# Kernel optimization log

Hardware: AMD Instinct MI355X
Metric: run time of the kernel (lower is better)

Reference implementation:

```python
import jax, jax.numpy as jnp
import numpy as np

HEADS = 8
DIM_HEAD = 64
SCALE = DIM_HEAD ** -0.5


def setup_inputs() -> dict:
    key = jax.random.key(0)
    ks = jax.random.split(key, 7)
    b, n, m = 2, 4096, 4096
    query_dim, context_dim, inner = 1024, 768, HEADS * DIM_HEAD
    s = 0.02
    return {
        "x": jax.random.normal(ks[0], (b, n, query_dim), jnp.float32),
        "context": jax.random.normal(ks[1], (b, m, context_dim), jnp.float32),
        "Wq": jax.random.normal(ks[2], (query_dim, inner), jnp.float32) * s,
        "Wk": jax.random.normal(ks[3], (context_dim, inner), jnp.float32) * s,
        "Wv": jax.random.normal(ks[4], (context_dim, inner), jnp.float32) * s,
        "Wo": jax.random.normal(ks[5], (inner, query_dim), jnp.float32) * s,
        "bo": jnp.zeros((query_dim,), jnp.float32),
    }


def reference(x, context, Wq, Wk, Wv, Wo, bo):
    b, n, _ = x.shape
    m = context.shape[1]
    # projections (no bias), split heads: b n (h d) -> b n h d
    q = (x @ Wq).reshape(b, n, HEADS, DIM_HEAD)
    k = (context @ Wk).reshape(b, m, HEADS, DIM_HEAD)
    v = (context @ Wv).reshape(b, m, HEADS, DIM_HEAD)
    # fp32 QK^T (ATTN_PRECISION='fp32' path), full [b,h,n,m] scores
    sim = jnp.einsum("bihd,bjhd->bhij", q.astype(jnp.float32), k.astype(jnp.float32)) * SCALE
    attn = jax.nn.softmax(sim, axis=-1).astype(v.dtype)
    out = jnp.einsum("bhij,bjhd->bihd", attn, v).reshape(b, n, HEADS * DIM_HEAD)
    # to_out: Linear with bias (dropout=0 is identity)
    return out @ Wo + bo
```

## Files before the change

### kernel.cpp

```cpp
#include <hip/hip_runtime.h>
#include <hip/hip_bf16.h>
#include <cmath>


using bf16_t = __hip_bfloat16;
typedef __bf16 bf16x8 __attribute__((ext_vector_type(8)));
typedef float  f32x4  __attribute__((ext_vector_type(4)));

static constexpr int BATCH = 2;
static constexpr int NQ    = 4096;
static constexpr int NKV   = 4096;
static constexpr int NH    = 8;
static constexpr int DH    = 64;
static constexpr int INNER = NH * DH;
static constexpr int QDIM  = 1024;
static constexpr int CDIM  = 768;
static constexpr float QSCALE = 0.125f * 1.4426950408889634f;

#define MFMA_BF16(a, b, c) __builtin_amdgcn_mfma_f32_16x16x32_bf16((a), (b), (c), 0, 0, 0)

__device__ __forceinline__ float fast_exp2(float x) {
  return __builtin_amdgcn_exp2f(x);
}

__device__ __forceinline__ void gload_lds16(const bf16_t* g, bf16_t* l) {
  __builtin_amdgcn_global_load_lds(
      (const __attribute__((address_space(1))) unsigned int*)(uintptr_t)g,
      (__attribute__((address_space(3))) unsigned int*)(unsigned int)(uintptr_t)l,
      16, 0, 0);
}

__global__ __launch_bounds__(256) void cast_kernel(const float* __restrict__ in,
                                                   bf16_t* __restrict__ out, int n8) {
  int id = blockIdx.x * 256 + threadIdx.x;
  if (id >= n8) return;
  float4 a = ((const float4*)in)[2 * id];
  float4 b = ((const float4*)in)[2 * id + 1];
  bf16_t t[8] = {__float2bfloat16(a.x), __float2bfloat16(a.y), __float2bfloat16(a.z),
                 __float2bfloat16(a.w), __float2bfloat16(b.x), __float2bfloat16(b.y),
                 __float2bfloat16(b.z), __float2bfloat16(b.w)};
  ((uint4*)out)[id] = *(const uint4*)t;
}

__global__ __launch_bounds__(256) void wtrans_kernel(const float* __restrict__ W,
                                                     bf16_t* __restrict__ WT,
                                                     int K, int N) {
  __shared__ float tile[32][33];
  const int bn = blockIdx.x * 32, bk = blockIdx.y * 32;
  const int tx = threadIdx.x & 31, ty = threadIdx.x >> 5;
  for (int yy = ty; yy < 32; yy += 8)
    tile[yy][tx] = W[(size_t)(bk + yy) * N + bn + tx];
  __syncthreads();
  for (int yy = ty; yy < 32; yy += 8)
    WT[(size_t)(bn + yy) * K + bk + tx] = __float2bfloat16(tile[tx][yy]);
}

template <int IM, int OUT_MODE>
__global__ __launch_bounds__(256) void gemm_kernel(const bf16_t* __restrict__ A,
                                                   const bf16_t* __restrict__ WT,
                                                   void* __restrict__ Cp,
                                                   void* __restrict__ Cp2,
                                                   const float* __restrict__ bias,
                                                   float ascale, int M, int N, int K) {
  constexpr int BM = IM * 32;
  __shared__ __align__(16) bf16_t As[BM][32];
  __shared__ __align__(16) bf16_t Bs[128][32];
  const int tid = threadIdx.x;
  const int lane = tid & 63, wave = tid >> 6;
  const int lane15 = lane & 15, quad = lane >> 4;
  const int wm = (wave >> 1) * (BM / 2), wn = (wave & 1) * 64;
  const int m0 = blockIdx.x * BM, n0 = blockIdx.y * 128;

  const f32x4 vzero = {0.f, 0.f, 0.f, 0.f};
  f32x4 acc[IM][4];
  for (int i = 0; i < IM; ++i)
    for (int j = 0; j < 4; ++j) acc[i][j] = vzero;

  const int crow = lane >> 2, ccol = (lane & 3) * 8;
  for (int k0 = 0; k0 < K; k0 += 32) {
    if constexpr (IM == 4) {
      for (int cc = 0; cc < 2; ++cc) {
        int c = wave * 2 + cc;
        gload_lds16(A + (size_t)(m0 + c * 16 + crow) * K + k0 + ccol, &As[c * 16][0]);
        gload_lds16(WT + (size_t)(n0 + c * 16 + crow) * K + k0 + ccol, &Bs[c * 16][0]);
      }
    } else {
      gload_lds16(A + (size_t)(m0 + wave * 16 + crow) * K + k0 + ccol, &As[wave * 16][0]);
      for (int cc = 0; cc < 2; ++cc) {
        int c = wave * 2 + cc;
        gload_lds16(WT + (size_t)(n0 + c * 16 + crow) * K + k0 + ccol, &Bs[c * 16][0]);
      }
    }
    __syncthreads();
    bf16x8 af[IM], bfr[4];
    for (int i = 0; i < IM; ++i)
      af[i] = *reinterpret_cast<const bf16x8*>(&As[wm + i * 16 + lane15][quad * 8]);
    for (int j = 0; j < 4; ++j)
      bfr[j] = *reinterpret_cast<const bf16x8*>(&Bs[wn + j * 16 + lane15][quad * 8]);
    for (int i = 0; i < IM; ++i)
      for (int j = 0; j < 4; ++j) acc[i][j] = MFMA_BF16(af[i], bfr[j], acc[i][j]);
    __syncthreads();
  }

  for (int i = 0; i < IM; ++i) {
    int gm = m0 + wm + i * 16 + quad * 4;
    for (int j = 0; j < 4; ++j) {
      int gn = n0 + wn + j * 16 + lane15;
      for (int r = 0; r < 4; ++r) {
        float v = acc[i][j][r];
        if constexpr (OUT_MODE == 0) {
          ((bf16_t*)Cp)[(size_t)(gm + r) * N + gn] = __float2bfloat16(v * ascale);
        } else if constexpr (OUT_MODE == 1) {
          ((float*)Cp)[(size_t)(gm + r) * N + gn] = v + bias[gn];
        } else {
          if (gn < INNER) {
            ((bf16_t*)Cp)[(size_t)(gm + r) * INNER + gn] = __float2bfloat16(v);
          } else {
            int gmr = gm + r;
            ((bf16_t*)Cp2)[((size_t)(gmr >> 12) * INNER + (gn - INNER)) * (size_t)NKV +
                           (gmr & 4095)] = __float2bfloat16(v);
          }
        }
      }
    }
  }
}

__global__ __launch_bounds__(256) void attn_kernel(const bf16_t* Qg ,
                                                   const bf16_t* __restrict__ Kg ,
                                                   const bf16_t* __restrict__ Vtg ,
                                                   bf16_t* Og ) {
  __shared__ __align__(16) bf16_t KsF[2][8][512];
  __shared__ __align__(16) bf16_t VtF[2][8][512];
  __shared__ __align__(16) bf16_t PsA[128][72];

  const int tid = threadIdx.x;
  const int lane = tid & 63, wave = tid >> 6;
  const int lane15 = lane & 15, quad = lane >> 4;
  const int wrow = wave * 32;
  const int q0 = blockIdx.x * 128;
  const int h = blockIdx.y;
  const int b = blockIdx.z;

  const size_t qbase  = ((size_t)b * NQ + q0) * INNER + h * DH;
  const size_t kbase  = ((size_t)b * NKV) * INNER + h * DH;
  const size_t vtbase = ((size_t)(b * NH + h) * DH) * NKV;

  bf16x8 qf[2][2];
  for (int i = 0; i < 2; ++i)
    for (int ks = 0; ks < 2; ++ks)
      qf[i][ks] = *reinterpret_cast<const bf16x8*>(
          Qg + qbase + (size_t)(wrow + i * 16 + lane15) * INNER + ks * 32 + quad * 8);

  const f32x4 vzero = {0.f, 0.f, 0.f, 0.f};
  f32x4 acc_o[2][4];
  float l_part[2] = {0.f, 0.f};
  for (int i = 0; i < 2; ++i)
    for (int j = 0; j < 4; ++j) acc_o[i][j] = vzero;

  const int c0 = wave * 2, c1 = wave * 2 + 1;
  auto kaddr = [&](int c, int kv0) {
    return Kg + kbase + (size_t)(kv0 + (c & 3) * 16 + lane15) * INNER + (c >> 2) * 32 + quad * 8;
  };
  auto vaddr = [&](int c, int kv0) {
    return Vtg + vtbase + (size_t)((c & 3) * 16 + lane15) * NKV + kv0 + (c >> 2) * 32 + quad * 8;
  };
  uint4 kr0 = *(const uint4*)kaddr(c0, 0), kr1 = *(const uint4*)kaddr(c1, 0);
  uint4 vr0 = *(const uint4*)vaddr(c0, 0), vr1 = *(const uint4*)vaddr(c1, 0);

  constexpr int T = NKV / 64;
  for (int t = 0; t < T; ++t) {
    const int cur = t & 1;
    *(uint4*)&KsF[cur][c0][lane * 8] = kr0;
    *(uint4*)&KsF[cur][c1][lane * 8] = kr1;
    *(uint4*)&VtF[cur][c0][lane * 8] = vr0;
    *(uint4*)&VtF[cur][c1][lane * 8] = vr1;
    __syncthreads();

    f32x4 acc_st[4][2];
    for (int j = 0; j < 4; ++j)
      for (int i = 0; i < 2; ++i) acc_st[j][i] = vzero;
    for (int ks = 0; ks < 2; ++ks) {
      bf16x8 kf[4];
      for (int j = 0; j < 4; ++j)
        kf[j] = *reinterpret_cast<const bf16x8*>(&KsF[cur][ks * 4 + j][lane * 8]);
      for (int j = 0; j < 4; ++j)
        for (int i = 0; i < 2; ++i) acc_st[j][i] = MFMA_BF16(kf[j], qf[i][ks], acc_st[j][i]);
    }

    if (t + 1 < T) {
      int kv0n = (t + 1) * 64;
      kr0 = *(const uint4*)kaddr(c0, kv0n);
      kr1 = *(const uint4*)kaddr(c1, kv0n);
      vr0 = *(const uint4*)vaddr(c0, kv0n);
      vr1 = *(const uint4*)vaddr(c1, kv0n);
    }

    for (int i = 0; i < 2; ++i) {
      for (int j = 0; j < 4; ++j) {
        bf16_t t4[4];
        for (int r = 0; r < 4; ++r) {
          float p = fast_exp2(acc_st[j][i][r]);
          l_part[i] += p;
          t4[r] = __float2bfloat16(p);
        }
        *(uint2*)&PsA[wrow + i * 16 + lane15][j * 16 + quad * 4] = *(const uint2*)t4;
      }
    }
    __syncthreads();

    for (int ks = 0; ks < 2; ++ks) {
      bf16x8 pf[2], vf[4];
      for (int i = 0; i < 2; ++i)
        pf[i] = *reinterpret_cast<const bf16x8*>(&PsA[wrow + i * 16 + lane15][ks * 32 + quad * 8]);
      for (int j = 0; j < 4; ++j)
        vf[j] = *reinterpret_cast<const bf16x8*>(&VtF[cur][ks * 4 + j][lane * 8]);
      for (int i = 0; i < 2; ++i)
        for (int j = 0; j < 4; ++j) acc_o[i][j] = MFMA_BF16(pf[i], vf[j], acc_o[i][j]);
    }
  }

  for (int i = 0; i < 2; ++i) {
    float l = l_part[i];
    l += __shfl_xor(l, 16, 64);
    l += __shfl_xor(l, 32, 64);
    float inv = 1.f / l;
    for (int r = 0; r < 4; ++r) {
      float invr = __shfl(inv, quad * 4 + r, 16);
      int row = wrow + i * 16 + quad * 4 + r;
      for (int j = 0; j < 4; ++j)
        Og[qbase + (size_t)row * INNER + j * 16 + lane15] =
            __float2bfloat16(acc_o[i][j][r] * invr);
    }
  }
}

extern "C" void kernel_launch(void* const* d_in, const int* in_sizes, int n_in,
                              void* d_out, int out_size, void* d_ws, size_t ws_size,
                              hipStream_t stream) {
  (void)in_sizes; (void)n_in; (void)out_size; (void)ws_size;
  const float* x   = (const float*)d_in[0];
  const float* ctx = (const float*)d_in[1];
  const float* Wq  = (const float*)d_in[2];
  const float* Wk  = (const float*)d_in[3];
  const float* Wv  = (const float*)d_in[4];
  const float* Wo  = (const float*)d_in[5];
  const float* bo  = (const float*)d_in[6];
  float* out = (float*)d_out;

  char* ws = (char*)d_ws;
  size_t off = 0;
  auto take = [&](size_t nelem) { bf16_t* p = (bf16_t*)(ws + off); off += nelem * 2; return p; };
  bf16_t* WqT  = take((size_t)INNER * QDIM);
  bf16_t* WkvT = take((size_t)(2 * INNER) * CDIM);
  bf16_t* WoT  = take((size_t)QDIM * INNER);
  bf16_t* qob  = take((size_t)BATCH * NQ * INNER);
  bf16_t* kb   = take((size_t)BATCH * NKV * INNER);
  bf16_t* vtb  = take((size_t)BATCH * INNER * NKV);

  bf16_t* xb   = (bf16_t*)d_out;
  bf16_t* ctxb = xb + (size_t)BATCH * NQ * QDIM;

  const int M = BATCH * NQ;
  const int xN8 = BATCH * NQ * QDIM / 8, cN8 = BATCH * NKV * CDIM / 8;

  cast_kernel<<<(xN8 + 255) / 256, 256, 0, stream>>>(x, xb, xN8);
  cast_kernel<<<(cN8 + 255) / 256, 256, 0, stream>>>(ctx, ctxb, cN8);
  wtrans_kernel<<<dim3(INNER / 32, QDIM / 32), 256, 0, stream>>>(Wq, WqT, QDIM, INNER);
  wtrans_kernel<<<dim3(INNER / 32, CDIM / 32), 256, 0, stream>>>(Wk, WkvT, CDIM, INNER);
  wtrans_kernel<<<dim3(INNER / 32, CDIM / 32), 256, 0, stream>>>(
      Wv, WkvT + (size_t)INNER * CDIM, CDIM, INNER);
  wtrans_kernel<<<dim3(QDIM / 32, INNER / 32), 256, 0, stream>>>(Wo, WoT, INNER, QDIM);

  gemm_kernel<2, 0><<<dim3(M / 64, INNER / 128), 256, 0, stream>>>(
      xb, WqT, qob, nullptr, nullptr, QSCALE, M, INNER, QDIM);
  gemm_kernel<4, 3><<<dim3(M / 128, (2 * INNER) / 128), 256, 0, stream>>>(
      ctxb, WkvT, kb, vtb, nullptr, 1.f, M, 2 * INNER, CDIM);

  attn_kernel<<<dim3(NQ / 128, NH, BATCH), 256, 0, stream>>>(qob, kb, vtb, qob);

  gemm_kernel<4, 1><<<dim3(M / 128, QDIM / 128), 256, 0, stream>>>(
      qob, WoT, out, nullptr, bo, 1.f, M, QDIM, INNER);
}
```

Baseline: 294.3 us.

## Use 8 waves of 16 query rows in attention and smaller GEMM tiles

The attention kernel now launches 512 threads per block, with each of 8 waves owning 16 query rows instead of 4 waves owning 32. Each wave now loads one K and one V chunk per tile instead of two. This halves per-wave register accumulators and should raise wave-level parallelism to better hide latency, at the cost of less Q-fragment reuse per wave. The KV and output-projection GEMMs switch to a 64-row tile variant, giving more blocks and better CU fill, at the cost of less reuse per tile.

```diff
diff --git a/kernel.cpp b/kernel.cpp
--- a/kernel.cpp
+++ b/kernel.cpp
@@ -126,7 +126,7 @@
   }
 }
 
-__global__ __launch_bounds__(256) void attn_kernel(const bf16_t* Qg ,
+__global__ __launch_bounds__(512) void attn_kernel(const bf16_t* Qg ,
                                                    const bf16_t* __restrict__ Kg ,
                                                    const bf16_t* __restrict__ Vtg ,
                                                    bf16_t* Og ) {
@@ -137,7 +137,7 @@
   const int tid = threadIdx.x;
   const int lane = tid & 63, wave = tid >> 6;
   const int lane15 = lane & 15, quad = lane >> 4;
-  const int wrow = wave * 32;
+  const int wrow = wave * 16;
   const int q0 = blockIdx.x * 128;
   const int h = blockIdx.y;
   const int b = blockIdx.z;
@@ -146,92 +146,78 @@
   const size_t kbase  = ((size_t)b * NKV) * INNER + h * DH;
   const size_t vtbase = ((size_t)(b * NH + h) * DH) * NKV;
 
-  bf16x8 qf[2][2];
-  for (int i = 0; i < 2; ++i)
-    for (int ks = 0; ks < 2; ++ks)
-      qf[i][ks] = *reinterpret_cast<const bf16x8*>(
-          Qg + qbase + (size_t)(wrow + i * 16 + lane15) * INNER + ks * 32 + quad * 8);
+  bf16x8 qf[2];
+  for (int ks = 0; ks < 2; ++ks)
+    qf[ks] = *reinterpret_cast<const bf16x8*>(
+        Qg + qbase + (size_t)(wrow + lane15) * INNER + ks * 32 + quad * 8);
 
   const f32x4 vzero = {0.f, 0.f, 0.f, 0.f};
-  f32x4 acc_o[2][4];
-  float l_part[2] = {0.f, 0.f};
-  for (int i = 0; i < 2; ++i)
-    for (int j = 0; j < 4; ++j) acc_o[i][j] = vzero;
-
-  const int c0 = wave * 2, c1 = wave * 2 + 1;
-  auto kaddr = [&](int c, int kv0) {
-    return Kg + kbase + (size_t)(kv0 + (c & 3) * 16 + lane15) * INNER + (c >> 2) * 32 + quad * 8;
+  f32x4 acc_o[4];
+  float l_part = 0.f;
+  for (int j = 0; j < 4; ++j) acc_o[j] = vzero;
+
+  const int cw = wave;
+  auto kaddr = [&](int kv0) {
+    return Kg + kbase + (size_t)(kv0 + (cw & 3) * 16 + lane15) * INNER + (cw >> 2) * 32 + quad * 8;
   };
-  auto vaddr = [&](int c, int kv0) {
-    return Vtg + vtbase + (size_t)((c & 3) * 16 + lane15) * NKV + kv0 + (c >> 2) * 32 + quad * 8;
+  auto vaddr = [&](int kv0) {
+    return Vtg + vtbase + (size_t)((cw & 3) * 16 + lane15) * NKV + kv0 + (cw >> 2) * 32 + quad * 8;
   };
-  uint4 kr0 = *(const uint4*)kaddr(c0, 0), kr1 = *(const uint4*)kaddr(c1, 0);
-  uint4 vr0 = *(const uint4*)vaddr(c0, 0), vr1 = *(const uint4*)vaddr(c1, 0);
+  uint4 kr = *(const uint4*)kaddr(0);
+  uint4 vr = *(const uint4*)vaddr(0);
 
   constexpr int T = NKV / 64;
   for (int t = 0; t < T; ++t) {
     const int cur = t & 1;
-    *(uint4*)&KsF[cur][c0][lane * 8] = kr0;
-    *(uint4*)&KsF[cur][c1][lane * 8] = kr1;
-    *(uint4*)&VtF[cur][c0][lane * 8] = vr0;
-    *(uint4*)&VtF[cur][c1][lane * 8] = vr1;
-    __syncthreads();
-
-    f32x4 acc_st[4][2];
-    for (int j = 0; j < 4; ++j)
-      for (int i = 0; i < 2; ++i) acc_st[j][i] = vzero;
+    *(uint4*)&KsF[cur][cw][lane * 8] = kr;
+    *(uint4*)&VtF[cur][cw][lane * 8] = vr;
+    __syncthreads();
+
+    f32x4 acc_st[4];
+    for (int j = 0; j < 4; ++j) acc_st[j] = vzero;
     for (int ks = 0; ks < 2; ++ks) {
       bf16x8 kf[4];
       for (int j = 0; j < 4; ++j)
         kf[j] = *reinterpret_cast<const bf16x8*>(&KsF[cur][ks * 4 + j][lane * 8]);
-      for (int j = 0; j < 4; ++j)
-        for (int i = 0; i < 2; ++i) acc_st[j][i] = MFMA_BF16(kf[j], qf[i][ks], acc_st[j][i]);
+      for (int j = 0; j < 4; ++j) acc_st[j] = MFMA_BF16(kf[j], qf[ks], acc_st[j]);
     }
 
     if (t + 1 < T) {
       int kv0n = (t + 1) * 64;
-      kr0 = *(const uint4*)kaddr(c0, kv0n);
-      kr1 = *(const uint4*)kaddr(c1, kv0n);
-      vr0 = *(const uint4*)vaddr(c0, kv0n);
-      vr1 = *(const uint4*)vaddr(c1, kv0n);
-    }
-
-    for (int i = 0; i < 2; ++i) {
-      for (int j = 0; j < 4; ++j) {
-        bf16_t t4[4];
-        for (int r = 0; r < 4; ++r) {
-          float p = fast_exp2(acc_st[j][i][r]);
-          l_part[i] += p;
-          t4[r] = __float2bfloat16(p);
-        }
-        *(uint2*)&PsA[wrow + i * 16 + lane15][j * 16 + quad * 4] = *(const uint2*)t4;
-      }
+      kr = *(const uint4*)kaddr(kv0n);
+      vr = *(const uint4*)vaddr(kv0n);
+    }
+
+    for (int j = 0; j < 4; ++j) {
+      bf16_t t4[4];
+      for (int r = 0; r < 4; ++r) {
+        float p = fast_exp2(acc_st[j][r]);
+        l_part += p;
+        t4[r] = __float2bfloat16(p);
+      }
+      *(uint2*)&PsA[wrow + lane15][j * 16 + quad * 4] = *(const uint2*)t4;
     }
     __syncthreads();
 
     for (int ks = 0; ks < 2; ++ks) {
-      bf16x8 pf[2], vf[4];
-      for (int i = 0; i < 2; ++i)
-        pf[i] = *reinterpret_cast<const bf16x8*>(&PsA[wrow + i * 16 + lane15][ks * 32 + quad * 8]);
+      bf16x8 pf, vf[4];
+      pf = *reinterpret_cast<const bf16x8*>(&PsA[wrow + lane15][ks * 32 + quad * 8]);
       for (int j = 0; j < 4; ++j)
         vf[j] = *reinterpret_cast<const bf16x8*>(&VtF[cur][ks * 4 + j][lane * 8]);
-      for (int i = 0; i < 2; ++i)
-        for (int j = 0; j < 4; ++j) acc_o[i][j] = MFMA_BF16(pf[i], vf[j], acc_o[i][j]);
-    }
-  }
-
-  for (int i = 0; i < 2; ++i) {
-    float l = l_part[i];
-    l += __shfl_xor(l, 16, 64);
-    l += __shfl_xor(l, 32, 64);
-    float inv = 1.f / l;
-    for (int r = 0; r < 4; ++r) {
-      float invr = __shfl(inv, quad * 4 + r, 16);
-      int row = wrow + i * 16 + quad * 4 + r;
-      for (int j = 0; j < 4; ++j)
-        Og[qbase + (size_t)row * INNER + j * 16 + lane15] =
-            __float2bfloat16(acc_o[i][j][r] * invr);
-    }
+      for (int j = 0; j < 4; ++j) acc_o[j] = MFMA_BF16(pf, vf[j], acc_o[j]);
+    }
+  }
+
+  float l = l_part;
+  l += __shfl_xor(l, 16, 64);
+  l += __shfl_xor(l, 32, 64);
+  float inv = 1.f / l;
+  for (int r = 0; r < 4; ++r) {
+    float invr = __shfl(inv, quad * 4 + r, 16);
+    int row = wrow + quad * 4 + r;
+    for (int j = 0; j < 4; ++j)
+      Og[qbase + (size_t)row * INNER + j * 16 + lane15] =
+          __float2bfloat16(acc_o[j][r] * invr);
   }
 }
 
@@ -274,11 +260,11 @@
 
   gemm_kernel<2, 0><<<dim3(M / 64, INNER / 128), 256, 0, stream>>>(
       xb, WqT, qob, nullptr, nullptr, QSCALE, M, INNER, QDIM);
-  gemm_kernel<4, 3><<<dim3(M / 128, (2 * INNER) / 128), 256, 0, stream>>>(
+  gemm_kernel<2, 3><<<dim3(M / 64, (2 * INNER) / 128), 256, 0, stream>>>(
       ctxb, WkvT, kb, vtb, nullptr, 1.f, M, 2 * INNER, CDIM);
 
-  attn_kernel<<<dim3(NQ / 128, NH, BATCH), 256, 0, stream>>>(qob, kb, vtb, qob);
-
-  gemm_kernel<4, 1><<<dim3(M / 128, QDIM / 128), 256, 0, stream>>>(
+  attn_kernel<<<dim3(NQ / 128, NH, BATCH), 512, 0, stream>>>(qob, kb, vtb, qob);
+
+  gemm_kernel<2, 1><<<dim3(M / 64, QDIM / 128), 256, 0, stream>>>(
       qob, WoT, out, nullptr, bo, 1.f, M, QDIM, INNER);
 }
```

New measurement: 280.4 us. 1.05x faster.
